# Kernel tuning notes

Measured on AMD Instinct MI355X. Metric: run time of the kernel, lower is better.

The kernel has to match this reference:

```python
import jax, jax.numpy as jnp
import numpy as np

B, K, NP = 2, 48, 25            # batch, context_length, grid_x*grid_y
C, H, L = 768, 12, 6            # n_embd, n_head, n_layer
COLORS, VOCAB, IS = 10, 40, 26  # color_num, vocab_size, intention_size
MAXT = 1000                     # max_timestep
TOK = NP + 4                    # tokens per timestep (rtg, 25 states, action, pnp, intention)
T = K * TOK                     # total sequence length


def layernorm(x, g, b, eps=1e-5):
    m = x.mean(-1, keepdims=True)
    v = ((x - m) ** 2).mean(-1, keepdims=True)
    return (x - m) * jax.lax.rsqrt(v + eps) * g + b


def causal_attn(x, wq, bq, wk, bk, wv, bv, wo, bo):
    Bx, Tx, Cx = x.shape
    hd = Cx // H
    def heads(w, bb):
        return (x @ w + bb).reshape(Bx, Tx, H, hd).transpose(0, 2, 1, 3)
    q, k, v = heads(wq, bq), heads(wk, bk), heads(wv, bv)
    att = jnp.einsum('bhqd,bhkd->bhqk', q, k) * (1.0 / np.sqrt(hd))
    mask = jnp.tril(jnp.ones((Tx, Tx), bool))
    att = jnp.where(mask, att, -jnp.inf)
    att = jax.nn.softmax(att, axis=-1)
    y = jnp.einsum('bhqk,bhkd->bhqd', att, v).transpose(0, 2, 1, 3).reshape(Bx, Tx, Cx)
    return y @ wo + bo


def setup_inputs() -> dict:
    key = jax.random.key(0)
    ks = iter(jax.random.split(key, 64))
    def nrm(shape):
        return jax.random.normal(next(ks), shape, jnp.float32) * 0.02
    inp = dict(
        states=jax.random.randint(next(ks), (B, K * NP), 0, COLORS),
        actions=jax.random.randint(next(ks), (B, K), 0, VOCAB),
        rtgs=jax.random.normal(next(ks), (B, K), jnp.float32),
        timesteps=jax.random.randint(next(ks), (B, K), 0, MAXT + 1),
        pnp=jax.random.normal(next(ks), (B, K, NP), jnp.float32),
        intentions=jax.random.randint(next(ks), (B, K, 2), 0, IS),
        pos_emb=nrm((K + 1, C)),               # (block_size, C)
        global_pos_emb=nrm((MAXT + 1, C)),
        state_tab=nrm((COLORS, C)),
        action_tab=nrm((VOCAB, C)),
        ret_W=nrm((1, C)), ret_b=jnp.zeros((C,)),
        pnp_W=nrm((NP, C)), pnp_b=jnp.zeros((C,)),
        src_tab=nrm((IS, C)), dst_tab=nrm((IS, C)),
        int_W=nrm((2 * C, C)), int_b=jnp.zeros((C,)),
        ln1_g=jnp.ones((L, C)), ln1_b=jnp.zeros((L, C)),
        ln2_g=jnp.ones((L, C)), ln2_b=jnp.zeros((L, C)),
        Wq=nrm((L, C, C)), bq=jnp.zeros((L, C)),
        Wk=nrm((L, C, C)), bk=jnp.zeros((L, C)),
        Wv=nrm((L, C, C)), bv=jnp.zeros((L, C)),
        Wo=nrm((L, C, C)), bo=jnp.zeros((L, C)),
        Wm1=nrm((L, C, 4 * C)), bm1=jnp.zeros((L, 4 * C)),
        Wm2=nrm((L, 4 * C, C)), bm2=jnp.zeros((L, C)),
        lnf_g=jnp.ones((C,)), lnf_b=jnp.zeros((C,)),
        Whs=nrm((C, COLORS)), bhs=jnp.zeros((COLORS,)),
        Wha=nrm((C, VOCAB)), bha=jnp.zeros((VOCAB,)),
        Whr=nrm((C, 1)), bhr=jnp.zeros((1,)),
        Whi=nrm((C, 2 * IS)), bhi=jnp.zeros((2 * IS,)),
    )
    return inp


def reference(states, actions, rtgs, timesteps, pnp, intentions,
              pos_emb, global_pos_emb, state_tab, action_tab,
              ret_W, ret_b, pnp_W, pnp_b, src_tab, dst_tab, int_W, int_b,
              ln1_g, ln1_b, ln2_g, ln2_b, Wq, bq, Wk, bk, Wv, bv, Wo, bo,
              Wm1, bm1, Wm2, bm2, lnf_g, lnf_b,
              Whs, bhs, Wha, bha, Whr, bhr, Whi, bhi):
    # --- embeddings, interleaved as [rtg, state_0..24, action, pnp, intention] per timestep ---
    st = state_tab[states].reshape(B, K, NP, C)                    # strided writes 1+i::TOK
    ae = action_tab[actions][:, :, None, :]
    re = (rtgs[..., None] @ ret_W + ret_b)[:, :, None, :]          # rtgs.unsqueeze(-1) -> Linear(1,C)
    pe = (pnp @ pnp_W + pnp_b)[:, :, None, :]
    ie_in = jnp.concatenate([src_tab[intentions[..., 0]], dst_tab[intentions[..., 1]]], axis=-1)
    ie = (ie_in @ int_W + int_b)[:, :, None, :]
    tok = jnp.concatenate([re, st, ae, pe, ie], axis=2).reshape(B, T, C)
    # --- positions: gather global + local pos_emb[:block_size-1], repeat_interleave by TOK ---
    pos = global_pos_emb[timesteps] + pos_emb[:K][None]            # (B, K, C)
    x = tok + jnp.repeat(pos, TOK, axis=1)
    # --- transformer stack (dropout p=0) ---
    def blk(h, p):
        l1g, l1b, l2g, l2b, wq, bq_, wk, bk_, wv, bv_, wo, bo_, w1, b1, w2, b2 = p
        h = h + causal_attn(layernorm(h, l1g, l1b), wq, bq_, wk, bk_, wv, bv_, wo, bo_)
        m = layernorm(h, l2g, l2b)
        h = h + jax.nn.gelu(m @ w1 + b1, approximate=False) @ w2 + b2
        return h, None
    x, _ = jax.lax.scan(blk, x, (ln1_g, ln1_b, ln2_g, ln2_b, Wq, bq, Wk, bk, Wv, bv, Wo, bo, Wm1, bm1, Wm2, bm2))
    x = layernorm(x, lnf_g, lnf_b)
    xr = x.reshape(B, K, TOK, C)
    logits = x @ Whs + bhs                                         # (B, T, COLORS)
    logit_action = xr[:, :, NP + 1] @ Wha + bha                    # (B, K, VOCAB)
    logit_rtg = (xr[:, :, 0] @ Whr + bhr)[..., 0]                  # (B, K)
    li = xr[:, :, NP + 3] @ Whi + bhi                              # (B, K, 2*IS)
    return logits, logit_action, logit_rtg, li[..., :IS], li[..., IS:]
```

## Files before the change

### kernel.cpp

```cpp
#include <hip/hip_runtime.h>
#include <hip/hip_bf16.h>
#include <math.h>


typedef __hip_bfloat16 bf16;
typedef __attribute__((ext_vector_type(4))) short s4v;
typedef __attribute__((ext_vector_type(8))) short s8v;
typedef __attribute__((ext_vector_type(4))) float f4v;
typedef unsigned int u32;

#define DEV static __device__ __forceinline__

constexpr int NBATCH = 2;
constexpr int NK   = 48;
constexpr int NNP  = 25;
constexpr int NC   = 768;
constexpr int NH   = 12;
constexpr int NL   = 6;
constexpr int NTOK = 29;
constexpr int NT   = NK * NTOK;
constexpr int NM   = NBATCH * NT;
constexpr int MPAD = 2816;

DEV float bs2f(short s) {
  unsigned u = ((unsigned)(unsigned short)s) << 16;
  float f; __builtin_memcpy(&f, &u, 4); return f;
}
DEV short f2bs(float f) {
  bf16 h = __float2bfloat16(f);
  short s; __builtin_memcpy(&s, &h, 2); return s;
}

DEV void async16(const short* g, short* l) {
  __builtin_amdgcn_global_load_lds(
      (const __attribute__((address_space(1))) u32*)g,
      (__attribute__((address_space(3))) u32*)l, 16, 0, 0);
}

__global__ __launch_bounds__(256) void transpose_kernel(
    const float* __restrict__ src, bf16* __restrict__ dst, int R, int C)
{
  int c0 = blockIdx.x * 32, r0 = blockIdx.y * 32;
  __shared__ float tl[32][33];
  int rr = threadIdx.x >> 5, cc = threadIdx.x & 31;
#pragma unroll
  for (int p = 0; p < 4; p++)
    tl[rr + p * 8][cc] = src[(long)(r0 + rr + p * 8) * C + c0 + cc];
  __syncthreads();
#pragma unroll
  for (int p = 0; p < 4; p++)
    dst[(long)(c0 + rr + p * 8) * R + r0 + cc] = __float2bfloat16(tl[cc][rr + p * 8]);
}

__global__ __launch_bounds__(256) void transpose_layer_kernel(
    const float* __restrict__ Wq, const float* __restrict__ Wk,
    const float* __restrict__ Wv, const float* __restrict__ Wo,
    const float* __restrict__ Wm1, const float* __restrict__ Wm2,
    bf16* __restrict__ WqkvT, bf16* __restrict__ WoT,
    bf16* __restrict__ Wm1T, bf16* __restrict__ Wm2T, int multi)
{
  int blk = blockIdx.x;
  int l = blk / 1728, t = blk - l * 1728;
  long so = (long)l * 768 * 768;
  long mo = (long)l * 768 * 3072;
  long dl = multi ? l : 0;
  const float* src; bf16* dst; int R, C, tile;
  if (t < 432) {
    int m = t / 144; tile = t - m * 144;
    src = (m == 0 ? Wq : (m == 1 ? Wk : Wv)) + so;
    dst = WqkvT + dl * (2304L * 768) + (long)m * 768 * 768; R = 768; C = 768;
  } else if (t < 576)  { src = Wo + so;  dst = WoT  + dl * (768L * 768);  tile = t - 432;  R = 768;  C = 768;  }
  else if (t < 1152)   { src = Wm1 + mo; dst = Wm1T + dl * (3072L * 768); tile = t - 576;  R = 768;  C = 3072; }
  else                 { src = Wm2 + mo; dst = Wm2T + dl * (768L * 3072); tile = t - 1152; R = 3072; C = 768;  }
  int ct = C / 64;
  int tr = tile / ct, tc = tile - tr * ct;
  int r0 = tr * 64, c0 = tc * 64;

  __shared__ short tl[64][66];
  int t4 = threadIdx.x & 15, rr = threadIdx.x >> 4;
#pragma unroll
  for (int p = 0; p < 4; p++) {
    int row = rr + p * 16;
    f4v v = *(const f4v*)(src + (long)(r0 + row) * C + c0 + t4 * 4);
    tl[t4 * 4 + 0][row] = f2bs(v.x);
    tl[t4 * 4 + 1][row] = f2bs(v.y);
    tl[t4 * 4 + 2][row] = f2bs(v.z);
    tl[t4 * 4 + 3][row] = f2bs(v.w);
  }
  __syncthreads();
#pragma unroll
  for (int p = 0; p < 4; p++) {
    int drow = rr + p * 16;
    s4v w = *(const s4v*)&tl[drow][t4 * 4];
    *(s4v*)((short*)dst + (long)(c0 + drow) * R + r0 + t4 * 4) = w;
  }
}

__global__ __launch_bounds__(256) void gather_ie_kernel(
    const int* __restrict__ intentions, const float* __restrict__ src_tab,
    const float* __restrict__ dst_tab, bf16* __restrict__ ie_in)
{
  int idx = blockIdx.x * 256 + threadIdx.x;
  if (idx >= 96 * 1536) return;
  int row = idx / 1536, col = idx - row * 1536;
  float v;
  if (col < 768) v = src_tab[intentions[row * 2 + 0] * 768 + col];
  else           v = dst_tab[intentions[row * 2 + 1] * 768 + col - 768];
  ie_in[idx] = __float2bfloat16(v);
}

__global__ __launch_bounds__(256) void embed_kernel(
    const int* __restrict__ states, const int* __restrict__ actions,
    const float* __restrict__ rtgs, const int* __restrict__ timesteps,
    const float* __restrict__ pnp,
    const float* __restrict__ pos_emb, const float* __restrict__ gpe,
    const float* __restrict__ state_tab, const float* __restrict__ action_tab,
    const float* __restrict__ retW, const float* __restrict__ retb,
    const float* __restrict__ pnpW, const float* __restrict__ pnpb,
    const bf16* __restrict__ ieb, float* __restrict__ X)
{
  int bk = blockIdx.x;
  int b = bk / NK, ts = bk - b * NK;
  int c = blockIdx.y * 256 + threadIdx.x;

  float rtg = rtgs[bk];
  int tstep = timesteps[bk];
  int act   = actions[bk];

  long base = (long)(b * NT + ts * NTOK) * NC;
  float pos = gpe[(long)tstep * NC + c] + pos_emb[ts * NC + c];

  X[base + c] = rtg * retW[c] + retb[c] + pos;
  const int* sp = states + bk * NNP;
#pragma unroll
  for (int i = 0; i < NNP; i++)
    X[base + (1 + i) * NC + c] = state_tab[sp[i] * NC + c] + pos;
  X[base + 26 * NC + c] = action_tab[act * NC + c] + pos;
  float ap = pnpb[c];
  const float* pv = pnp + bk * NNP;
#pragma unroll
  for (int i = 0; i < NNP; i++) ap += pv[i] * pnpW[i * NC + c];
  X[base + 27 * NC + c] = ap + pos;
  X[base + 28 * NC + c] = __bfloat162float(ieb[bk * NC + c]) + pos;
}

__global__ __launch_bounds__(256) void ln_kernel(
    const float* __restrict__ X, bf16* __restrict__ XN,
    const float* __restrict__ g, const float* __restrict__ bt)
{
  int row = blockIdx.x, tid = threadIdx.x;
  const float* x = X + (long)row * NC;
  float v0 = x[tid], v1 = x[tid + 256], v2 = x[tid + 512];
  float s = v0 + v1 + v2;
#pragma unroll
  for (int o = 32; o > 0; o >>= 1) s += __shfl_down(s, o, 64);
  __shared__ float red[8];
  if ((tid & 63) == 0) red[tid >> 6] = s;
  __syncthreads();
  float mean = (red[0] + red[1] + red[2] + red[3]) * (1.0f / NC);
  float d0 = v0 - mean, d1 = v1 - mean, d2 = v2 - mean;
  float qq = d0 * d0 + d1 * d1 + d2 * d2;
#pragma unroll
  for (int o = 32; o > 0; o >>= 1) qq += __shfl_down(qq, o, 64);
  __syncthreads();
  if ((tid & 63) == 0) red[tid >> 6] = qq;
  __syncthreads();
  float var = (red[0] + red[1] + red[2] + red[3]) * (1.0f / NC);
  float rs = 1.0f / sqrtf(var + 1e-5f);
  bf16* xn = XN + (long)row * NC;
  xn[tid      ] = __float2bfloat16(d0 * rs * g[tid      ] + bt[tid      ]);
  xn[tid + 256] = __float2bfloat16(d1 * rs * g[tid + 256] + bt[tid + 256]);
  xn[tid + 512] = __float2bfloat16(d2 * rs * g[tid + 512] + bt[tid + 512]);
}

template<int BM, int BN>
__global__ __launch_bounds__(256) void gemm_kernel(
    const bf16* __restrict__ A, const bf16* __restrict__ WT,
    const float* __restrict__ b0, const float* __restrict__ b1,
    const float* __restrict__ b2, int Nsplit,
    bf16* __restrict__ outb, float* __restrict__ resid,
    int M, int N, int K, int flags)
{
  constexpr int IM  = BM / 64;
  constexpr int JN  = BN / 16;
  constexpr int ACH = BM / 64;
  constexpr int BCH = BN / 64;
  __shared__ __align__(1024) short As[2][BM * 32];
  __shared__ __align__(1024) short Bs[2][BN * 32];

  int tid = threadIdx.x, wave = tid >> 6, lane = tid & 63;
  int quad = lane >> 4, l16 = lane & 15;
  int m0 = blockIdx.y * BM, n0 = blockIdx.x * BN;
  int wm = wave * (BM / 4);
  int lr = lane >> 2, lc = (lane & 3) * 8;

  const short* Ag = (const short*)A + (long)m0 * K + lc;
  const short* Bg = (const short*)WT + (long)n0 * K + lc;

  const short* ag[ACH]; int alo[ACH];
#pragma unroll
  for (int c = 0; c < ACH; c++) {
    int rbase = wave * (16 * ACH) + c * 16;
    ag[c] = Ag + (long)(rbase + lr) * K;
    alo[c] = rbase * 32;
  }
  const short* bg[BCH]; int blo[BCH];
#pragma unroll
  for (int c = 0; c < BCH; c++) {
    int rbase = wave * (16 * BCH) + c * 16;
    bg[c] = Bg + (long)(rbase + lr) * K;
    blo[c] = rbase * 32;
  }

  f4v zero4 = {0.f, 0.f, 0.f, 0.f};
  f4v acc[IM][JN];
#pragma unroll
  for (int i = 0; i < IM; i++)
#pragma unroll
    for (int j = 0; j < JN; j++) acc[i][j] = zero4;

  int nk = K >> 5;
#pragma unroll
  for (int c = 0; c < ACH; c++) async16(ag[c], &As[0][alo[c]]);
#pragma unroll
  for (int c = 0; c < BCH; c++) async16(bg[c], &Bs[0][blo[c]]);
  __syncthreads();

  for (int kt = 0; kt < nk; kt++) {
    int cur = kt & 1, nxt = cur ^ 1;
    if (kt + 1 < nk) {
      int ko = (kt + 1) << 5;
#pragma unroll
      for (int c = 0; c < ACH; c++) async16(ag[c] + ko, &As[nxt][alo[c]]);
#pragma unroll
      for (int c = 0; c < BCH; c++) async16(bg[c] + ko, &Bs[nxt][blo[c]]);
    }
    s8v af[IM], bf8[JN];
#pragma unroll
    for (int i = 0; i < IM; i++) {
      const short* p = &As[cur][(wm + i * 16 + l16) * 32 + quad * 8];
      af[i].lo = *(const s4v*)p; af[i].hi = *(const s4v*)(p + 4);
    }
#pragma unroll
    for (int j = 0; j < JN; j++) {
      const short* p = &Bs[cur][(j * 16 + l16) * 32 + quad * 8];
      bf8[j].lo = *(const s4v*)p; bf8[j].hi = *(const s4v*)(p + 4);
    }
#pragma unroll
    for (int i = 0; i < IM; i++)
#pragma unroll
      for (int j = 0; j < JN; j++)
        acc[i][j] = __builtin_amdgcn_mfma_f32_16x16x32_bf16(af[i], bf8[j], acc[i][j], 0, 0, 0);
    __syncthreads();
  }

#pragma unroll
  for (int i = 0; i < IM; i++) {
    int rbase = m0 + wm + i * 16 + quad * 4;
#pragma unroll
    for (int j = 0; j < JN; j++) {
      int bc = n0 + j * 16;
      int wsel = bc / Nsplit;
      const float* bp = wsel == 0 ? b0 : (wsel == 1 ? b1 : b2);
      float bv = bp[bc - wsel * Nsplit + l16];
      int col = bc + l16;
#pragma unroll
      for (int r = 0; r < 4; r++) {
        int row = rbase + r;
        if (row < M) {
          float v = acc[i][j][r] + bv;
          if (flags & 1) v = 0.5f * v * (1.0f + erff(v * 0.70710678118654752f));
          if (flags & 2) resid[(long)row * N + col] += v;
          else outb[(long)row * N + col] = __float2bfloat16(v);
        }
      }
    }
  }
}

constexpr int ASTR = 72;

__global__ __launch_bounds__(256) void attn_kernel(
    const bf16* __restrict__ QKV, bf16* __restrict__ Yg)
{
  int qt = blockIdx.x, h = blockIdx.y, b = blockIdx.z;
  int q0 = qt * 64;
  int tid = threadIdx.x, wave = tid >> 6, lane = tid & 63, quad = lane >> 4, l16 = lane & 15;

  __shared__ short Qs[64 * ASTR];
  __shared__ short Ks[64 * ASTR];
  __shared__ short Vt[64 * ASTR];
  __shared__ short Ps[64 * ASTR];

  int r = tid >> 2, c16 = (tid & 3) * 16;
  const short* src = (const short*)QKV;
  s8v zz = {0,0,0,0,0,0,0,0};

  s8v qv0 = zz, qv1 = zz;
  if (q0 + r < NT) {
    const s8v* p = (const s8v*)(src + (long)(b * NT + q0 + r) * 2304 + h * 64 + c16);
    qv0 = p[0]; qv1 = p[1];
  }
  {
    short* qp = &Qs[r * ASTR + c16];
    *(s4v*)(qp    ) = qv0.lo; *(s4v*)(qp + 4) = qv0.hi;
    *(s4v*)(qp + 8) = qv1.lo; *(s4v*)(qp + 12) = qv1.hi;
  }

  f4v zero4 = {0.f, 0.f, 0.f, 0.f};
  f4v Of[4];
#pragma unroll
  for (int j = 0; j < 4; j++) Of[j] = zero4;
  float m_r[4], l_r[4];
#pragma unroll
  for (int rg = 0; rg < 4; rg++) { m_r[rg] = -1e30f; l_r[rg] = 0.f; }

  int kend = q0 + 63; if (kend > NT - 1) kend = NT - 1;

  s8v kv0 = zz, kv1 = zz, vv0 = zz, vv1 = zz;
  if (r < NT) {
    const s8v* pk = (const s8v*)(src + (long)(b * NT + r) * 2304 + 768 + h * 64 + c16);
    kv0 = pk[0]; kv1 = pk[1];
    const s8v* pvv = (const s8v*)(src + (long)(b * NT + r) * 2304 + 1536 + h * 64 + c16);
    vv0 = pvv[0]; vv1 = pvv[1];
  }

  for (int k0 = 0; k0 <= kend; k0 += 64) {
    __syncthreads();
    {
      short* kp = &Ks[r * ASTR + c16];
      *(s4v*)(kp    ) = kv0.lo; *(s4v*)(kp + 4) = kv0.hi;
      *(s4v*)(kp + 8) = kv1.lo; *(s4v*)(kp + 12) = kv1.hi;
      short* vt = &Vt[c16 * ASTR + r];
      vt[ 0 * ASTR] = vv0.s0; vt[ 1 * ASTR] = vv0.s1; vt[ 2 * ASTR] = vv0.s2; vt[ 3 * ASTR] = vv0.s3;
      vt[ 4 * ASTR] = vv0.s4; vt[ 5 * ASTR] = vv0.s5; vt[ 6 * ASTR] = vv0.s6; vt[ 7 * ASTR] = vv0.s7;
      vt[ 8 * ASTR] = vv1.s0; vt[ 9 * ASTR] = vv1.s1; vt[10 * ASTR] = vv1.s2; vt[11 * ASTR] = vv1.s3;
      vt[12 * ASTR] = vv1.s4; vt[13 * ASTR] = vv1.s5; vt[14 * ASTR] = vv1.s6; vt[15 * ASTR] = vv1.s7;
    }
    __syncthreads();

    int k1 = k0 + 64;
    s8v nk0 = zz, nk1 = zz, nv0 = zz, nv1 = zz;
    if (k1 <= kend && k1 + r < NT) {
      const s8v* pk = (const s8v*)(src + (long)(b * NT + k1 + r) * 2304 + 768 + h * 64 + c16);
      nk0 = pk[0]; nk1 = pk[1];
      const s8v* pvv = (const s8v*)(src + (long)(b * NT + k1 + r) * 2304 + 1536 + h * 64 + c16);
      nv0 = pvv[0]; nv1 = pvv[1];
    }

    f4v sa[4];
#pragma unroll
    for (int j = 0; j < 4; j++) sa[j] = zero4;
#pragma unroll
    for (int ks = 0; ks < 2; ks++) {
      const short* pa = &Qs[(wave * 16 + l16) * ASTR + ks * 32 + quad * 8];
      s8v aq; aq.lo = *(const s4v*)pa; aq.hi = *(const s4v*)(pa + 4);
#pragma unroll
      for (int j = 0; j < 4; j++) {
        const short* pb = &Ks[(j * 16 + l16) * ASTR + ks * 32 + quad * 8];
        s8v bk8; bk8.lo = *(const s4v*)pb; bk8.hi = *(const s4v*)(pb + 4);
        sa[j] = __builtin_amdgcn_mfma_f32_16x16x32_bf16(aq, bk8, sa[j], 0, 0, 0);
      }
    }

#pragma unroll
    for (int j = 0; j < 4; j++) {
#pragma unroll
      for (int rg = 0; rg < 4; rg++) {
        int gq = q0 + wave * 16 + quad * 4 + rg;
        int gk = k0 + j * 16 + l16;
        sa[j][rg] = (gk <= gq && gq < NT) ? sa[j][rg] * 0.125f : -1e30f;
      }
    }

#pragma unroll
    for (int rg = 0; rg < 4; rg++) {
      float mx = fmaxf(fmaxf(sa[0][rg], sa[1][rg]), fmaxf(sa[2][rg], sa[3][rg]));
      mx = fmaxf(mx, __shfl_xor(mx, 1));
      mx = fmaxf(mx, __shfl_xor(mx, 2));
      mx = fmaxf(mx, __shfl_xor(mx, 4));
      mx = fmaxf(mx, __shfl_xor(mx, 8));
      float mn = fmaxf(m_r[rg], mx);
      float al = __expf(m_r[rg] - mn);
      m_r[rg] = mn;
      float ps = 0.f;
#pragma unroll
      for (int j = 0; j < 4; j++) {
        float e = __expf(sa[j][rg] - mn);
        sa[j][rg] = e;
        ps += e;
      }
      ps += __shfl_xor(ps, 1);
      ps += __shfl_xor(ps, 2);
      ps += __shfl_xor(ps, 4);
      ps += __shfl_xor(ps, 8);
      l_r[rg] = l_r[rg] * al + ps;
#pragma unroll
      for (int j = 0; j < 4; j++) Of[j][rg] *= al;
    }

#pragma unroll
    for (int j = 0; j < 4; j++)
#pragma unroll
      for (int rg = 0; rg < 4; rg++)
        Ps[(wave * 16 + quad * 4 + rg) * ASTR + j * 16 + l16] = f2bs(sa[j][rg]);
    __syncthreads();

#pragma unroll
    for (int ks = 0; ks < 2; ks++) {
      const short* pa = &Ps[(wave * 16 + l16) * ASTR + ks * 32 + quad * 8];
      s8v ap8; ap8.lo = *(const s4v*)pa; ap8.hi = *(const s4v*)(pa + 4);
#pragma unroll
      for (int j = 0; j < 4; j++) {
        const short* pb = &Vt[(j * 16 + l16) * ASTR + ks * 32 + quad * 8];
        s8v vp8; vp8.lo = *(const s4v*)pb; vp8.hi = *(const s4v*)(pb + 4);
        Of[j] = __builtin_amdgcn_mfma_f32_16x16x32_bf16(ap8, vp8, Of[j], 0, 0, 0);
      }
    }

    kv0 = nk0; kv1 = nk1; vv0 = nv0; vv1 = nv1;
  }

#pragma unroll
  for (int rg = 0; rg < 4; rg++) {
    int rloc = wave * 16 + quad * 4 + rg;
    int gq = q0 + rloc;
    if (gq < NT) {
      float inv = 1.0f / l_r[rg];
#pragma unroll
      for (int j = 0; j < 4; j++) {
        float ov = Of[j][rg] * inv;
        Yg[(long)(b * NT + gq) * NC + h * 64 + j * 16 + l16] = __float2bfloat16(ov);
      }
    }
  }
}

__global__ __launch_bounds__(256) void head_logits_kernel(
    const bf16* __restrict__ XN, const float* __restrict__ Whs,
    const float* __restrict__ bhs, float* __restrict__ out)
{
  int idx = blockIdx.x * 256 + threadIdx.x;
  if (idx >= NM * 10) return;
  int row = idx / 10, n = idx - row * 10;
  const short* x = (const short*)XN + (long)row * NC;
  float a0 = bhs[n], a1 = 0.f, a2 = 0.f, a3 = 0.f;
  for (int k = 0; k < NC; k += 4) {
    a0 += bs2f(x[k    ]) * Whs[(k    ) * 10 + n];
    a1 += bs2f(x[k + 1]) * Whs[(k + 1) * 10 + n];
    a2 += bs2f(x[k + 2]) * Whs[(k + 2) * 10 + n];
    a3 += bs2f(x[k + 3]) * Whs[(k + 3) * 10 + n];
  }
  out[idx] = a0 + a1 + a2 + a3;
}

__global__ __launch_bounds__(128) void head_small_kernel(
    const bf16* __restrict__ XN,
    const float* __restrict__ Wha, const float* __restrict__ bha,
    const float* __restrict__ Whr, const float* __restrict__ bhr,
    const float* __restrict__ Whi, const float* __restrict__ bhi,
    float* __restrict__ outA, float* __restrict__ outR,
    float* __restrict__ outS, float* __restrict__ outD)
{
  int blk = blockIdx.x;
  int b = blk / NK, ts = blk - b * NK;
  int tid = threadIdx.x;
  if (tid >= 93) return;
  const short* xs = (const short*)XN;
  if (tid < 40) {
    long row = (long)(b * NT + ts * NTOK + 26) * NC;
    float a0 = bha[tid], a1 = 0.f, a2 = 0.f, a3 = 0.f;
    for (int k = 0; k < NC; k += 4) {
      a0 += bs2f(xs[row + k    ]) * Wha[(k    ) * 40 + tid];
      a1 += bs2f(xs[row + k + 1]) * Wha[(k + 1) * 40 + tid];
      a2 += bs2f(xs[row + k + 2]) * Wha[(k + 2) * 40 + tid];
      a3 += bs2f(xs[row + k + 3]) * Wha[(k + 3) * 40 + tid];
    }
    outA[blk * 40 + tid] = a0 + a1 + a2 + a3;
  } else if (tid == 40) {
    long row = (long)(b * NT + ts * NTOK) * NC;
    float a0 = bhr[0], a1 = 0.f, a2 = 0.f, a3 = 0.f;
    for (int k = 0; k < NC; k += 4) {
      a0 += bs2f(xs[row + k    ]) * Whr[k    ];
      a1 += bs2f(xs[row + k + 1]) * Whr[k + 1];
      a2 += bs2f(xs[row + k + 2]) * Whr[k + 2];
      a3 += bs2f(xs[row + k + 3]) * Whr[k + 3];
    }
    outR[blk] = a0 + a1 + a2 + a3;
  } else {
    int n = tid - 41;
    long row = (long)(b * NT + ts * NTOK + 28) * NC;
    float a0 = bhi[n], a1 = 0.f, a2 = 0.f, a3 = 0.f;
    for (int k = 0; k < NC; k += 4) {
      a0 += bs2f(xs[row + k    ]) * Whi[(k    ) * 52 + n];
      a1 += bs2f(xs[row + k + 1]) * Whi[(k + 1) * 52 + n];
      a2 += bs2f(xs[row + k + 2]) * Whi[(k + 2) * 52 + n];
      a3 += bs2f(xs[row + k + 3]) * Whi[(k + 3) * 52 + n];
    }
    if (n < 26) outS[blk * 26 + n] = a0 + a1 + a2 + a3;
    else        outD[blk * 26 + (n - 26)] = a0 + a1 + a2 + a3;
  }
}

extern "C" void kernel_launch(void* const* d_in, const int* in_sizes, int n_in,
                              void* d_out, int out_size, void* d_ws, size_t ws_size,
                              hipStream_t stream)
{
  (void)in_sizes; (void)n_in; (void)out_size;

  const int*   states     = (const int*)  d_in[0];
  const int*   actions    = (const int*)  d_in[1];
  const float* rtgs       = (const float*)d_in[2];
  const int*   timesteps  = (const int*)  d_in[3];
  const float* pnp        = (const float*)d_in[4];
  const int*   intentions = (const int*)  d_in[5];
  const float* pos_emb    = (const float*)d_in[6];
  const float* gpe        = (const float*)d_in[7];
  const float* state_tab  = (const float*)d_in[8];
  const float* action_tab = (const float*)d_in[9];
  const float* retW  = (const float*)d_in[10];
  const float* retb  = (const float*)d_in[11];
  const float* pnpW  = (const float*)d_in[12];
  const float* pnpb  = (const float*)d_in[13];
  const float* src_tab = (const float*)d_in[14];
  const float* dst_tab = (const float*)d_in[15];
  const float* intW  = (const float*)d_in[16];
  const float* intb  = (const float*)d_in[17];
  const float* ln1g  = (const float*)d_in[18];
  const float* ln1b  = (const float*)d_in[19];
  const float* ln2g  = (const float*)d_in[20];
  const float* ln2b  = (const float*)d_in[21];
  const float* Wq = (const float*)d_in[22];
  const float* bq = (const float*)d_in[23];
  const float* Wk = (const float*)d_in[24];
  const float* bk = (const float*)d_in[25];
  const float* Wv = (const float*)d_in[26];
  const float* bv = (const float*)d_in[27];
  const float* Wo = (const float*)d_in[28];
  const float* bo = (const float*)d_in[29];
  const float* Wm1 = (const float*)d_in[30];
  const float* bm1 = (const float*)d_in[31];
  const float* Wm2 = (const float*)d_in[32];
  const float* bm2 = (const float*)d_in[33];
  const float* lnfg = (const float*)d_in[34];
  const float* lnfb = (const float*)d_in[35];
  const float* Whs = (const float*)d_in[36];
  const float* bhs = (const float*)d_in[37];
  const float* Wha = (const float*)d_in[38];
  const float* bha = (const float*)d_in[39];
  const float* Whr = (const float*)d_in[40];
  const float* bhr = (const float*)d_in[41];
  const float* Whi = (const float*)d_in[42];
  const float* bhi = (const float*)d_in[43];

  char* wsb = (char*)d_ws;
  float* X   = (float*)(wsb);
  bf16* XN   = (bf16*)(wsb + 8650752);
  bf16* QKVb = (bf16*)(wsb + 12976128);
  bf16* Yb   = (bf16*)(wsb + 25952256);
  bf16* H1   = QKVb;
  bf16* WTbase = (bf16*)(wsb + 30277632);

  const size_t NEED_BIG = 30277632UL + 84934656UL + 2949120UL;
  bool big = ws_size >= NEED_BIG;

  long sQKV = 2304L * 768, sO = 768L * 768, sM1 = 3072L * 768, sM2 = 768L * 3072;
  bf16 *WqkvT, *WoT, *Wm1T, *Wm2T, *intWT;
  if (big) {
    WqkvT = WTbase;
    WoT   = WqkvT + 6 * sQKV;
    Wm1T  = WoT   + 6 * sO;
    Wm2T  = Wm1T  + 6 * sM1;
    intWT = Wm2T  + 6 * sM2;
  } else {
    WqkvT = WTbase;
    WoT   = WqkvT + sQKV;
    Wm1T  = WoT + sO;
    Wm2T  = Wm1T + sM1;
    intWT = WTbase;
  }
  bf16* ie_in = intWT + 768L * 1536;
  bf16* ieb   = ie_in + 128L * 1536;

  float* out0 = (float*)d_out;
  float* out1 = out0 + 27840;
  float* out2 = out1 + 3840;
  float* out3 = out2 + 96;
  float* out4 = out3 + 2496;

  transpose_kernel<<<dim3(24, 48), 256, 0, stream>>>(intW, intWT, 1536, 768);
  gather_ie_kernel<<<(96 * 1536 + 255) / 256, 256, 0, stream>>>(intentions, src_tab, dst_tab, ie_in);
  gemm_kernel<64, 64><<<dim3(12, 2), 256, 0, stream>>>(ie_in, intWT, intb, intb, intb, 768,
      ieb, nullptr, 96, 768, 1536, 0);
  embed_kernel<<<dim3(96, 3), 256, 0, stream>>>(
      states, actions, rtgs, timesteps, pnp, pos_emb, gpe, state_tab, action_tab,
      retW, retb, pnpW, pnpb, ieb, X);

  if (big)
    transpose_layer_kernel<<<1728 * NL, 256, 0, stream>>>(
        Wq, Wk, Wv, Wo, Wm1, Wm2, WqkvT, WoT, Wm1T, Wm2T, 1);

  for (int l = 0; l < NL; l++) {
    const long wofs = (long)l * NC * NC;
    const long mofs = (long)l * NC * 4 * NC;
    if (!big)
      transpose_layer_kernel<<<1728, 256, 0, stream>>>(
          Wq + wofs, Wk + wofs, Wv + wofs, Wo + wofs, Wm1 + mofs, Wm2 + mofs,
          WqkvT, WoT, Wm1T, Wm2T, 0);
    bf16* wqkv = big ? WqkvT + l * sQKV : WqkvT;
    bf16* wo   = big ? WoT   + l * sO   : WoT;
    bf16* wm1  = big ? Wm1T  + l * sM1  : Wm1T;
    bf16* wm2  = big ? Wm2T  + l * sM2  : Wm2T;

    ln_kernel<<<NM, 256, 0, stream>>>(X, XN, ln1g + l * NC, ln1b + l * NC);
    gemm_kernel<128, 64><<<dim3(36, 22), 256, 0, stream>>>(XN, wqkv,
        bq + l * NC, bk + l * NC, bv + l * NC, 768, QKVb, nullptr, NM, 2304, NC, 0);
    attn_kernel<<<dim3(22, NH, NBATCH), 256, 0, stream>>>(QKVb, Yb);
    gemm_kernel<64, 64><<<dim3(12, 44), 256, 0, stream>>>(Yb, wo,
        bo + l * NC, bo + l * NC, bo + l * NC, 768, nullptr, X, NM, 768, NC, 2);
    ln_kernel<<<NM, 256, 0, stream>>>(X, XN, ln2g + l * NC, ln2b + l * NC);
    gemm_kernel<128, 64><<<dim3(48, 22), 256, 0, stream>>>(XN, wm1,
        bm1 + l * 4 * NC, bm1 + l * 4 * NC, bm1 + l * 4 * NC, 4 * NC, H1, nullptr,
        NM, 3072, NC, 1);
    gemm_kernel<64, 64><<<dim3(12, 44), 256, 0, stream>>>(H1, wm2,
        bm2 + l * NC, bm2 + l * NC, bm2 + l * NC, 768, nullptr, X, NM, 768, 4 * NC, 2);
  }
  ln_kernel<<<NM, 256, 0, stream>>>(X, XN, lnfg, lnfb);
  head_logits_kernel<<<(NM * 10 + 255) / 256, 256, 0, stream>>>(XN, Whs, bhs, out0);
  head_small_kernel<<<NBATCH * NK, 128, 0, stream>>>(XN, Wha, bha, Whr, bhr, Whi, bhi,
      out1, out2, out3, out4);
}
```

Baseline: 1.624 ms.

## Triple-buffer GEMM shared-memory tiles with explicit vmcnt waits

Moves the GEMM K-loop from double to triple buffering in LDS, issuing async global loads two tiles ahead. Loads are tracked with explicit s_waitcnt vmcnt counts and raw barriers instead of __syncthreads, so one iteration's loads can stay in flight while the current tile is computed. The cost is 50% more shared memory per block, which may reduce occupancy. Correctness depends on the hard-coded vmcnt literals matching the number of async loads issued per stage.

```diff
diff --git a/kernel.cpp b/kernel.cpp
--- a/kernel.cpp
+++ b/kernel.cpp
@@ -10,6 +10,7 @@
 typedef unsigned int u32;
 
 #define DEV static __device__ __forceinline__
+#define VMCNT_ASM(n) asm volatile("s_waitcnt vmcnt(" #n ")" ::: "memory")
 
 constexpr int NBATCH = 2;
 constexpr int NK   = 48;
@@ -185,8 +186,10 @@
   constexpr int JN  = BN / 16;
   constexpr int ACH = BM / 64;
   constexpr int BCH = BN / 64;
-  __shared__ __align__(1024) short As[2][BM * 32];
-  __shared__ __align__(1024) short Bs[2][BN * 32];
+  constexpr int SC  = ACH + BCH;
+  static_assert(SC == 2 || SC == 3, "vmcnt literal dispatch");
+  __shared__ __align__(1024) short As[3][BM * 32];
+  __shared__ __align__(1024) short Bs[3][BN * 32];
 
   int tid = threadIdx.x, wave = tid >> 6, lane = tid & 63;
   int quad = lane >> 4, l16 = lane & 15;
@@ -220,20 +223,33 @@
     for (int j = 0; j < JN; j++) acc[i][j] = zero4;
 
   int nk = K >> 5;
+
 #pragma unroll
   for (int c = 0; c < ACH; c++) async16(ag[c], &As[0][alo[c]]);
 #pragma unroll
   for (int c = 0; c < BCH; c++) async16(bg[c], &Bs[0][blo[c]]);
-  __syncthreads();
+  if (nk > 1) {
+    int ko = 32;
+#pragma unroll
+    for (int c = 0; c < ACH; c++) async16(ag[c] + ko, &As[1][alo[c]]);
+#pragma unroll
+    for (int c = 0; c < BCH; c++) async16(bg[c] + ko, &Bs[1][blo[c]]);
+    if constexpr (SC == 2) VMCNT_ASM(2); else VMCNT_ASM(3);
+  } else {
+    VMCNT_ASM(0);
+  }
+  __builtin_amdgcn_s_barrier();
+  __builtin_amdgcn_sched_barrier(0);
 
   for (int kt = 0; kt < nk; kt++) {
-    int cur = kt & 1, nxt = cur ^ 1;
-    if (kt + 1 < nk) {
-      int ko = (kt + 1) << 5;
-#pragma unroll
-      for (int c = 0; c < ACH; c++) async16(ag[c] + ko, &As[nxt][alo[c]]);
-#pragma unroll
-      for (int c = 0; c < BCH; c++) async16(bg[c] + ko, &Bs[nxt][blo[c]]);
+    int cur = kt % 3;
+    if (kt + 2 < nk) {
+      int nb = (kt + 2) % 3;
+      int ko = (kt + 2) << 5;
+#pragma unroll
+      for (int c = 0; c < ACH; c++) async16(ag[c] + ko, &As[nb][alo[c]]);
+#pragma unroll
+      for (int c = 0; c < BCH; c++) async16(bg[c] + ko, &Bs[nb][blo[c]]);
     }
     s8v af[IM], bf8[JN];
 #pragma unroll
@@ -251,7 +267,12 @@
 #pragma unroll
       for (int j = 0; j < JN; j++)
         acc[i][j] = __builtin_amdgcn_mfma_f32_16x16x32_bf16(af[i], bf8[j], acc[i][j], 0, 0, 0);
-    __syncthreads();
+    if (kt + 1 < nk) {
+      if (kt + 2 < nk) { if constexpr (SC == 2) VMCNT_ASM(2); else VMCNT_ASM(3); }
+      else             { VMCNT_ASM(0); }
+      __builtin_amdgcn_s_barrier();
+      __builtin_amdgcn_sched_barrier(0);
+    }
   }
 
 #pragma unroll
```

Result: slower. 1.720 ms (+5.9%).
